# Kernel tuning notes

Measured on AMD Instinct MI355X. Metric: run time of the kernel, lower is better.

The kernel has to match this reference:

```python
import jax, jax.numpy as jnp
import numpy as np
from jax import lax

H = 1024  # hidden_size
L = 2     # num_layers


def gru_cell(x, h, Wih, Whh, bih, bhh):
    # PyTorch GRU gate order: r, z, n
    gi = x @ Wih.T + bih          # [B, 3H]
    gh = h @ Whh.T + bhh          # [B, 3H]
    ir, iz, inn = jnp.split(gi, 3, axis=-1)
    hr, hz, hn = jnp.split(gh, 3, axis=-1)
    r = jax.nn.sigmoid(ir + hr)
    z = jax.nn.sigmoid(iz + hz)
    n = jnp.tanh(inn + r * hn)
    return (1.0 - z) * n + z * h


def stacked_step(h, x_t, layers):
    # h: [L, B, H]; x_t: [B, in]; layers: list of (Wih, Whh, bih, bhh)
    hs = []
    inp = x_t
    for l, (Wih, Whh, bih, bhh) in enumerate(layers):
        hl = gru_cell(inp, h[l], Wih, Whh, bih, bhh)
        hs.append(hl)
        inp = hl
    return jnp.stack(hs), inp  # new hidden stack, top-layer output


def run_gru_seq(x_seq, h0, layers):
    # x_seq: [B, S, in] -> scan over time
    def step(h, x_t):
        h_new, out = stacked_step(h, x_t, layers)
        return h_new, out
    h_final, outs = lax.scan(step, h0, jnp.transpose(x_seq, (1, 0, 2)))
    return outs[-1], h_final  # last-timestep top-layer output [B, H]


def setup_inputs() -> dict:
    key = jax.random.key(0)
    ks = jax.random.split(key, 10)
    B, S = 128, 256

    def xavier(k, shape):
        fan_out, fan_in = shape
        std = np.sqrt(2.0 / (fan_in + fan_out))
        return jax.random.normal(k, shape, dtype=jnp.float32) * std

    inp = {
        "x": jax.random.normal(ks[0], (B, S), dtype=jnp.float32),
        "h0": jax.random.uniform(ks[1], (L, B, H), dtype=jnp.float32) * 0.01,
        "Wih0": xavier(ks[2], (3 * H, 1)),
        "Whh0": xavier(ks[3], (3 * H, H)),
        "bih0": jnp.zeros((3 * H,), jnp.float32),
        "bhh0": jnp.zeros((3 * H,), jnp.float32),
        "Wih1": xavier(ks[4], (3 * H, H)),
        "Whh1": xavier(ks[5], (3 * H, H)),
        "bih1": jnp.zeros((3 * H,), jnp.float32),
        "bhh1": jnp.zeros((3 * H,), jnp.float32),
        "fc_w": jax.random.uniform(ks[6], (1, H), jnp.float32, -1.0 / np.sqrt(H), 1.0 / np.sqrt(H)),
        "fc_b": jax.random.uniform(ks[7], (1,), jnp.float32, -1.0 / np.sqrt(H), 1.0 / np.sqrt(H)),
        "forcast_length": 8,
    }
    return inp


def reference(x, h0, Wih0, Whh0, bih0, bhh0, Wih1, Whh1, bih1, bhh1, fc_w, fc_b, forcast_length):
    layers = [(Wih0, Whh0, bih0, bhh0), (Wih1, Whh1, bih1, bhh1)]

    # forecast step i=0: full conditioning sequence
    out0, h = run_gru_seq(x[..., None], h0, layers)   # [B, H], [L, B, H]
    y0 = out0 @ fc_w.T + fc_b                          # [B, 1]

    def fstep(carry, _):
        xc, hc = carry                                 # xc: [B, 1]
        h_new, out = stacked_step(hc, xc, layers)
        y = out @ fc_w.T + fc_b                        # [B, 1]
        return (y, h_new), y[:, 0]

    (y_last, h_final), ys = lax.scan(fstep, (y0, h), None, length=forcast_length - 1)
    forcast_out = jnp.concatenate([y0[:, 0][None, :], ys], axis=0)  # [F, B]
    return jnp.mean(forcast_out, axis=0), h_final
```

## Files before the change

kernel.cpp:

```cpp
#include <hip/hip_runtime.h>

#define NB 128
#define NH 1024
#define NS 256
#define NF 8
#define NBLK 192
#define NTH 512
#define AG  __HIP_MEMORY_SCOPE_AGENT

#define GLOBL 0
#define RELL  64
#define INITL 128
#define XCNT  192
#define XARR  512
#define XCPY  1024

typedef _Float16 half_t;
typedef _Float16 f16x8 __attribute__((ext_vector_type(8)));
typedef float f32x4 __attribute__((ext_vector_type(4)));
typedef unsigned long long u64;

struct GP {
    const float *x, *hin, *Wih0, *Whh0, *bih0, *bhh0, *Wih1, *Whh1, *bih1, *bhh1, *fcw, *fcb;
    float *gib0, *gib1, *ys, *out;
    half_t *h0b0, *h0b1, *h1b0, *h1b1;
    char *reg;
    unsigned *bar;
};

__device__ __forceinline__ float fast_sigmoid(float x) { return 1.0f / (1.0f + __expf(-x)); }
__device__ __forceinline__ float fast_tanh(float x) {
    float e = __expf(2.0f * x);
    return (e - 1.0f) / (e + 1.0f);
}

__device__ __forceinline__ u64 ldu64(const void* p) {
    return __hip_atomic_load((const u64*)p, __ATOMIC_RELAXED, AG);
}
__device__ __forceinline__ void stu64(void* p, u64 v) {
    __hip_atomic_store((u64*)p, v, __ATOMIC_RELAXED, AG);
}
__device__ __forceinline__ float ldf32(const float* p) {
    return __hip_atomic_load(p, __ATOMIC_RELAXED, AG);
}
__device__ __forceinline__ unsigned aadd(unsigned* p, unsigned v) {
    return __hip_atomic_fetch_add(p, v, __ATOMIC_RELAXED, AG);
}
__device__ __forceinline__ unsigned ald(const unsigned* p) {
    return __hip_atomic_load(p, __ATOMIC_RELAXED, AG);
}

__device__ __forceinline__ void l2add(unsigned* p, unsigned v) {
    asm volatile("global_atomic_add %0, %1, off" :: "v"(p), "v"(v) : "memory");
}
__device__ __forceinline__ unsigned l2add_rtn(unsigned* p, unsigned v) {
    unsigned ret;
    asm volatile("global_atomic_add %0, %1, %2, off sc0\n\ts_waitcnt vmcnt(0)"
                 : "=v"(ret) : "v"(p), "v"(v) : "memory");
    return ret;
}

__global__ void k_init(const float* __restrict__ hin, half_t* __restrict__ h0h,
                       half_t* __restrict__ h1h, const float* __restrict__ fcb,
                       float* __restrict__ ys) {
    int i = blockIdx.x * 256 + threadIdx.x;
    h0h[i] = (half_t)hin[i];
    h1h[i] = (half_t)hin[NB * NH + i];
    if (blockIdx.x == 0) {
        float fb = fcb[0];
        for (int j = threadIdx.x; j < NF * NB; j += 256) ys[j] = fb;
    }
}

__global__ __launch_bounds__(NTH)
void k_gru(GP p) {
    extern __shared__ char lds[];
    const int tid = threadIdx.x;
    const int l   = tid & 63;
    const int wv  = tid >> 6;
    const int bid = blockIdx.x;
    const int role = (bid < 64) ? 0 : (bid < 128 ? 1 : 2);
    const int bc   = bid & 63;
    const int colbase = bc * 16;
    float* hl  = (float*)(lds + 98304);
    int* meta  = (int*)(lds + 106496);
    unsigned* bar = p.bar;

    {
        const float* Wsrc = (role == 0) ? p.Whh0 : ((role == 1) ? p.Wih1 : p.Whh1);
        for (int i = tid; i < 12288; i += NTH) {
            int row = i >> 8, j = i & 255;
            int g = row >> 4, r = row & 15;
            float4 v = *(const float4*)(Wsrc + (size_t)(g * NH + colbase + r) * NH + j * 4);
            union { half_t h[4]; uint2 u; } cv;
            cv.h[0] = (half_t)v.x; cv.h[1] = (half_t)v.y;
            cv.h[2] = (half_t)v.z; cv.h[3] = (half_t)v.w;
            *(uint2*)(lds + (row * 2048 + ((j * 8) ^ ((row & 7) << 4)))) = cv.u;
        }
        if (role != 1) {
            const float* hsrc = p.hin + (role == 2 ? NB * NH : 0);
            for (int i = tid; i < NB * 16; i += NTH) {
                int b = i >> 4, cl = i & 15;
                hl[i] = hsrc[(size_t)b * NH + colbase + cl];
            }
        }
    }

    if (tid == 0) {
        unsigned x;
        asm volatile("s_getreg_b32 %0, hwreg(HW_REG_XCC_ID)" : "=s"(x));
        x &= 7;
        unsigned r = aadd(bar + XCNT + x * 32, 1u);
        asm volatile("s_waitcnt vmcnt(0)" ::: "memory");
        aadd(bar + INITL, 1u);
        while (ald(bar + INITL) < NBLK) __builtin_amdgcn_s_sleep(1);
        int nn = 0, cnt = 0;
        for (int k = 0; k < 8; ++k) {
            unsigned c = ald(bar + XCNT + k * 32);
            if (c) ++cnt;
            if (k == (int)x) nn = (int)c;
        }
        meta[0] = (int)x; meta[1] = (int)r; meta[2] = nn; meta[3] = cnt;
    }
    __syncthreads();
    const int xcd_  = meta[0];
    const int rank_ = meta[1];
    const int n_    = meta[2];
    const int nx_   = meta[3];

    const int cloc = l & 15;
    const int c = colbase + cloc;
    float bi_[3] = {0,0,0}, bh_[3] = {0,0,0}, wx_[3] = {0,0,0}, fcwv = 0.f;
    if (role == 0) {
        #pragma unroll
        for (int g = 0; g < 3; ++g) {
            bi_[g] = p.bih0[g * NH + c]; bh_[g] = p.bhh0[g * NH + c];
            wx_[g] = p.Wih0[g * NH + c];
        }
    } else if (role == 2) {
        #pragma unroll
        for (int g = 0; g < 3; ++g) {
            bi_[g] = p.bih1[g * NH + c]; bh_[g] = p.bhh1[g * NH + c];
        }
        fcwv = p.fcw[c];
    }

    const int rbase[3] = { cloc * 2048, (16 + cloc) * 2048, (32 + cloc) * 2048 };
    const int rmask = (cloc & 7) << 4;
    const int kb0 = (l >> 4) << 4;
    const int arow = wv * 16 + cloc;
    const int b0base = wv * 16 + ((l >> 4) << 2);
    const int aloff = (l >> 4) * 2048 + arow * 16;

    auto gbar = [&](unsigned t) {
        __syncthreads();
        if (tid == 0) {
            l2add(bar + XARR + xcd_ * 32, 1u);
            if (rank_ == 0) {
                while (l2add_rtn(bar + XARR + xcd_ * 32, 0u) < (unsigned)n_ * t)
                    __builtin_amdgcn_s_sleep(1);
                unsigned old = aadd(bar + GLOBL, 1u);
                if (old == (unsigned)nx_ * t - 1u) aadd(bar + RELL, 1u);
            }
            while (ald(bar + RELL) < t) __builtin_amdgcn_s_sleep(1);
        }
        __syncthreads();
        asm volatile("buffer_inv" ::: "memory");
    };

    auto xcopy = [&](const half_t* h0s, const half_t* h1s, int slot) {
        char* dst = p.reg + ((size_t)(xcd_ * 2 + slot)) * 524288;
        for (int idx = rank_ * 512 + tid; idx < 32768; idx += n_ * 512) {
            int which = idx >> 14, kq = (idx >> 7) & 127, row = idx & 127;
            const half_t* s = (which ? h1s : h0s) + row * 1024 + kq * 8;
            union { u64 u[2]; uint4 v; } t;
            t.u[0] = ldu64(s);
            t.u[1] = ldu64(s + 4);
            *(uint4*)(dst + which * 262144 + (size_t)(kq * 128 + row) * 16) = t.v;
        }
    };
    auto csync = [&](unsigned ct) {
        __syncthreads();
        if (tid == 0) {
            l2add(bar + XCPY + xcd_ * 32, 1u);
            while (l2add_rtn(bar + XCPY + xcd_ * 32, 0u) < (unsigned)n_ * ct)
                __builtin_amdgcn_s_sleep(1);
        }
        __syncthreads();
    };

    auto do_gemm = [&](const char* regA, f32x4 (&acc)[3]) {
        const char* ap = regA + aloff;
        #pragma unroll 8
        for (int ks = 0; ks < 32; ++ks) {
            f16x8 a = *(const f16x8*)(ap + (size_t)ks * 8192);
            int kb = ks * 64 + kb0;
            #pragma unroll
            for (int g = 0; g < 3; ++g) {
                f16x8 bf = *(const f16x8*)(lds + rbase[g] + (kb ^ rmask));
                acc[g] = __builtin_amdgcn_mfma_f32_16x16x32_f16(a, bf, acc[g], 0, 0, 0);
            }
        }
    };

    auto pack_store_h = [&](half_t* hw, int b, float hn) {
        unsigned v = (unsigned)__builtin_bit_cast(unsigned short, (half_t)hn);
        unsigned o = __shfl_xor(v, 1);
        unsigned pair = (l & 1) ? (o | (v << 16)) : (v | (o << 16));
        unsigned p2 = __shfl_xor(pair, 2);
        u64 quad = (l & 2) ? (((u64)pair << 32) | p2) : ((u64)pair | ((u64)p2 << 32));
        if ((l & 3) == 0) stu64(hw + (size_t)b * NH + (c & ~3), quad);
    };

    auto l0_epi = [&](const float xv[4], f32x4 (&acc)[3], half_t* hw) {
        #pragma unroll
        for (int q = 0; q < 4; ++q) {
            int b = b0base + q;
            float gh0 = acc[0][q] + bh_[0];
            float gh1 = acc[1][q] + bh_[1];
            float gh2 = acc[2][q] + bh_[2];
            float r_ = fast_sigmoid(xv[q] * wx_[0] + bi_[0] + gh0);
            float z_ = fast_sigmoid(xv[q] * wx_[1] + bi_[1] + gh1);
            float n_2 = fast_tanh(xv[q] * wx_[2] + bi_[2] + r_ * gh2);
            float hp = hl[b * 16 + cloc];
            float hn = (1.0f - z_) * n_2 + z_ * hp;
            hl[b * 16 + cloc] = hn;
            pack_store_h(hw, b, hn);
        }
    };

    auto gi_epi = [&](f32x4 (&acc)[3], float* gw) {
        #pragma unroll
        for (int g = 0; g < 3; ++g) {
            union { f32x4 v; u64 u[2]; } t; t.v = acc[g];
            float* dst = gw + ((size_t)g * NH + c) * NB + b0base;
            stu64(dst, t.u[0]);
            stu64(dst + 2, t.u[1]);
        }
    };

    auto gh_epi = [&](f32x4 (&acc)[3], const f32x4 gv[3], half_t* hw, float* ydst) {
        float hn4[4];
        #pragma unroll
        for (int q = 0; q < 4; ++q) {
            int b = b0base + q;
            float gh0 = acc[0][q] + bh_[0];
            float gh1 = acc[1][q] + bh_[1];
            float gh2 = acc[2][q] + bh_[2];
            float r_ = fast_sigmoid(gv[0][q] + bi_[0] + gh0);
            float z_ = fast_sigmoid(gv[1][q] + bi_[1] + gh1);
            float n_2 = fast_tanh(gv[2][q] + bi_[2] + r_ * gh2);
            float hp = hl[b * 16 + cloc];
            float hn = (1.0f - z_) * n_2 + z_ * hp;
            hl[b * 16 + cloc] = hn;
            hn4[q] = hn;
            pack_store_h(hw, b, hn);
        }
        if (ydst) {
            float s0 = hn4[0] * fcwv, s1 = hn4[1] * fcwv, s2 = hn4[2] * fcwv, s3 = hn4[3] * fcwv;
            #pragma unroll
            for (int m = 1; m < 16; m <<= 1) {
                s0 += __shfl_xor(s0, m); s1 += __shfl_xor(s1, m);
                s2 += __shfl_xor(s2, m); s3 += __shfl_xor(s3, m);
            }
            if (cloc == 0) {
                atomicAdd(ydst + b0base, s0);
                atomicAdd(ydst + b0base + 1, s1);
                atomicAdd(ydst + b0base + 2, s2);
                atomicAdd(ydst + b0base + 3, s3);
            }
        }
    };

    auto load_gi = [&](const float* gr, f32x4 (&gv)[3]) {
        #pragma unroll
        for (int g = 0; g < 3; ++g) {
            union { f32x4 v; u64 u[2]; } t;
            const float* src = gr + ((size_t)g * NH + c) * NB + b0base;
            t.u[0] = ldu64(src);
            t.u[1] = ldu64(src + 2);
            gv[g] = t.v;
        }
    };

    unsigned tgt = 0, ctgt = 0;
    int cur0 = 0, cur1 = 0, gcur = 0;
    f32x4 zero4 = {0.f, 0.f, 0.f, 0.f};

    auto COPY = [&]() {
        ++ctgt;
        int slot = (int)(ctgt & 1);
        xcopy(cur0 ? p.h0b1 : p.h0b0, cur1 ? p.h1b1 : p.h1b0, slot);
        csync(ctgt);
        return p.reg + ((size_t)(xcd_ * 2 + slot)) * 524288;
    };

    for (int ph = 0; ph < NS + 2; ++ph) {
        const char* regB = COPY();
        if (role == 0 && ph < NS) {
            float xv[4];
            #pragma unroll
            for (int q = 0; q < 4; ++q) xv[q] = ldf32(p.x + (size_t)(b0base + q) * NS + ph);
            f32x4 acc[3] = {zero4, zero4, zero4};
            do_gemm(regB, acc);
            l0_epi(xv, acc, cur0 ? p.h0b0 : p.h0b1);
        } else if (role == 1 && ph >= 1 && ph <= NS) {
            f32x4 acc[3] = {zero4, zero4, zero4};
            do_gemm(regB, acc);
            gi_epi(acc, gcur ? p.gib0 : p.gib1);
        } else if (role == 2 && ph >= 2) {
            f32x4 gv[3];
            load_gi(gcur ? p.gib1 : p.gib0, gv);
            f32x4 acc[3] = {zero4, zero4, zero4};
            do_gemm(regB + 262144, acc);
            gh_epi(acc, gv, cur1 ? p.h1b0 : p.h1b1, (ph == NS + 1) ? p.ys : nullptr);
        }
        ++tgt; gbar(tgt);
        if (ph < NS) cur0 ^= 1;
        if (ph >= 1 && ph <= NS) gcur ^= 1;
        if (ph >= 2) cur1 ^= 1;
    }

    for (int i = 1; i < NF; ++i) {
        const char* regB = COPY();
        if (role == 0) {
            float xv[4];
            #pragma unroll
            for (int q = 0; q < 4; ++q) xv[q] = ldf32(p.ys + (i - 1) * NB + b0base + q);
            f32x4 acc[3] = {zero4, zero4, zero4};
            do_gemm(regB, acc);
            l0_epi(xv, acc, cur0 ? p.h0b0 : p.h0b1);
        }
        ++tgt; gbar(tgt); cur0 ^= 1;

        regB = COPY();
        if (role == 1) {
            f32x4 acc[3] = {zero4, zero4, zero4};
            do_gemm(regB, acc);
            gi_epi(acc, gcur ? p.gib0 : p.gib1);
        }
        ++tgt; gbar(tgt); gcur ^= 1;

        regB = COPY();
        if (role == 2) {
            f32x4 gv[3];
            load_gi(gcur ? p.gib1 : p.gib0, gv);
            f32x4 acc[3] = {zero4, zero4, zero4};
            do_gemm(regB + 262144, acc);
            gh_epi(acc, gv, cur1 ? p.h1b0 : p.h1b1, p.ys + i * NB);
        }
        ++tgt; gbar(tgt); cur1 ^= 1;
    }

    if (bid == 0 && tid < NB) {
        float s = 0.0f;
        #pragma unroll
        for (int k = 0; k < NF; ++k) s += ldf32(p.ys + k * NB + tid);
        p.out[tid] = s * 0.125f;
    }
    if (role != 1) {
        float* ob = p.out + NB + (role == 2 ? (size_t)NB * NH : 0);
        for (int i = tid; i < NB * 16; i += NTH) {
            int b = i >> 4, cl = i & 15;
            ob[(size_t)b * NH + colbase + cl] = hl[i];
        }
    }
}

extern "C" void kernel_launch(void* const* d_in, const int* in_sizes, int n_in,
                              void* d_out, int out_size, void* d_ws, size_t ws_size,
                              hipStream_t stream)
{
    GP p;
    p.x    = (const float*)d_in[0];
    p.hin  = (const float*)d_in[1];
    p.Wih0 = (const float*)d_in[2];
    p.Whh0 = (const float*)d_in[3];
    p.bih0 = (const float*)d_in[4];
    p.bhh0 = (const float*)d_in[5];
    p.Wih1 = (const float*)d_in[6];
    p.Whh1 = (const float*)d_in[7];
    p.bih1 = (const float*)d_in[8];
    p.bhh1 = (const float*)d_in[9];
    p.fcw  = (const float*)d_in[10];
    p.fcb  = (const float*)d_in[11];
    p.out  = (float*)d_out;

    char* ws = (char*)d_ws;
    p.bar  = (unsigned*)ws;                      ws += 8192;
    p.h0b0 = (half_t*)ws;                        ws += 262144;
    p.h0b1 = (half_t*)ws;                        ws += 262144;
    p.h1b0 = (half_t*)ws;                        ws += 262144;
    p.h1b1 = (half_t*)ws;                        ws += 262144;
    p.gib0 = (float*)ws;                         ws += 1572864;
    p.gib1 = (float*)ws;                         ws += 1572864;
    p.ys   = (float*)ws;                         ws += 4096;
    ws = (char*)(((size_t)ws + 4095) & ~(size_t)4095);
    p.reg  = ws;                                 ws += 8 * 2 * 524288;

    hipMemsetAsync(p.bar, 0, 8192, stream);
    k_init<<<512, 256, 0, stream>>>(p.hin, p.h0b0, p.h1b0, p.fcb, p.ys);

    void* args[] = { &p };
    if (hipLaunchCooperativeKernel((void*)k_gru, dim3(NBLK), dim3(NTH), args,
                                   106752, stream) != hipSuccess) {
        (void)hipGetLastError();
        k_gru<<<dim3(NBLK), dim3(NTH), 106752, stream>>>(p);
    }
}
```

Baseline: 3.316 ms.

## Restructure grid barrier release per XCD and streamline h-state staging copy

The global barrier now releases each XCD through a per-XCD counter: the XCD leader spins on the global count and then bumps a local release flag, so other blocks no longer all poll one global line. The staging copy becomes a straight linear memcpy with four batched non-temporal dwordx4 loads issued before any store, and the A-operand addressing in the GEMM is changed to match the new row-major staging layout. Loads of x and of the gi buffer are hoisted ahead of the copy and sync so their latency overlaps them. This adds explicit vmcnt waits before each barrier and assumes the buffer layout used by the GEMM is consistent with the unpermuted copy.

```diff
diff --git a/kernel.cpp b/kernel.cpp
--- a/kernel.cpp
+++ b/kernel.cpp
@@ -9,10 +9,10 @@
 #define AG  __HIP_MEMORY_SCOPE_AGENT
 
 #define GLOBL 0
-#define RELL  64
 #define INITL 128
 #define XCNT  192
 #define XARR  512
+#define XREL  768
 #define XCPY  1024
 
 typedef _Float16 half_t;
@@ -150,19 +150,24 @@
     const int kb0 = (l >> 4) << 4;
     const int arow = wv * 16 + cloc;
     const int b0base = wv * 16 + ((l >> 4) << 2);
-    const int aloff = (l >> 4) * 2048 + arow * 16;
+    const int aloff = arow * 2048 + ((l >> 4) << 4);
 
     auto gbar = [&](unsigned t) {
+        asm volatile("s_waitcnt vmcnt(0)" ::: "memory");
         __syncthreads();
         if (tid == 0) {
             l2add(bar + XARR + xcd_ * 32, 1u);
             if (rank_ == 0) {
                 while (l2add_rtn(bar + XARR + xcd_ * 32, 0u) < (unsigned)n_ * t)
                     __builtin_amdgcn_s_sleep(1);
-                unsigned old = aadd(bar + GLOBL, 1u);
-                if (old == (unsigned)nx_ * t - 1u) aadd(bar + RELL, 1u);
-            }
-            while (ald(bar + RELL) < t) __builtin_amdgcn_s_sleep(1);
+                aadd(bar + GLOBL, 1u);
+                while (aadd(bar + GLOBL, 0u) < (unsigned)nx_ * t)
+                    __builtin_amdgcn_s_sleep(1);
+                l2add(bar + XREL + xcd_ * 32, 1u);
+            } else {
+                while (l2add_rtn(bar + XREL + xcd_ * 32, 0u) < t)
+                    __builtin_amdgcn_s_sleep(1);
+            }
         }
         __syncthreads();
         asm volatile("buffer_inv" ::: "memory");
@@ -170,16 +175,28 @@
 
     auto xcopy = [&](const half_t* h0s, const half_t* h1s, int slot) {
         char* dst = p.reg + ((size_t)(xcd_ * 2 + slot)) * 524288;
-        for (int idx = rank_ * 512 + tid; idx < 32768; idx += n_ * 512) {
-            int which = idx >> 14, kq = (idx >> 7) & 127, row = idx & 127;
-            const half_t* s = (which ? h1s : h0s) + row * 1024 + kq * 8;
-            union { u64 u[2]; uint4 v; } t;
-            t.u[0] = ldu64(s);
-            t.u[1] = ldu64(s + 4);
-            *(uint4*)(dst + which * 262144 + (size_t)(kq * 128 + row) * 16) = t.v;
-        }
+        const int base = rank_ * NTH + tid;
+        const int stride = n_ * NTH;
+        uint4 v0, v1, v2, v3;
+        int i0 = base, i1 = base + stride, i2 = base + 2 * stride, i3 = base + 3 * stride;
+        const char* s0 = (i0 < 16384) ? (const char*)h0s + (size_t)i0 * 16 : (const char*)h1s + (size_t)(i0 - 16384) * 16;
+        const char* s1 = (i1 < 16384) ? (const char*)h0s + (size_t)i1 * 16 : (const char*)h1s + (size_t)(i1 - 16384) * 16;
+        const char* s2 = (i2 < 16384) ? (const char*)h0s + (size_t)i2 * 16 : (const char*)h1s + (size_t)(i2 - 16384) * 16;
+        const char* s3 = (i3 < 16384) ? (const char*)h0s + (size_t)i3 * 16 : (const char*)h1s + (size_t)(i3 - 16384) * 16;
+        if (i0 < 32768) asm volatile("global_load_dwordx4 %0, %1, off sc0 sc1" : "=v"(v0) : "v"(s0) : "memory");
+        if (i1 < 32768) asm volatile("global_load_dwordx4 %0, %1, off sc0 sc1" : "=v"(v1) : "v"(s1) : "memory");
+        if (i2 < 32768) asm volatile("global_load_dwordx4 %0, %1, off sc0 sc1" : "=v"(v2) : "v"(s2) : "memory");
+        if (i3 < 32768) asm volatile("global_load_dwordx4 %0, %1, off sc0 sc1" : "=v"(v3) : "v"(s3) : "memory");
+        __builtin_amdgcn_sched_barrier(0);
+        asm volatile("s_waitcnt vmcnt(0)" ::: "memory");
+        __builtin_amdgcn_sched_barrier(0);
+        if (i0 < 32768) *(uint4*)(dst + (size_t)i0 * 16) = v0;
+        if (i1 < 32768) *(uint4*)(dst + (size_t)i1 * 16) = v1;
+        if (i2 < 32768) *(uint4*)(dst + (size_t)i2 * 16) = v2;
+        if (i3 < 32768) *(uint4*)(dst + (size_t)i3 * 16) = v3;
     };
     auto csync = [&](unsigned ct) {
+        asm volatile("s_waitcnt vmcnt(0)" ::: "memory");
         __syncthreads();
         if (tid == 0) {
             l2add(bar + XCPY + xcd_ * 32, 1u);
@@ -193,7 +210,7 @@
         const char* ap = regA + aloff;
         #pragma unroll 8
         for (int ks = 0; ks < 32; ++ks) {
-            f16x8 a = *(const f16x8*)(ap + (size_t)ks * 8192);
+            f16x8 a = *(const f16x8*)(ap + ks * 64);
             int kb = ks * 64 + kb0;
             #pragma unroll
             for (int g = 0; g < 3; ++g) {
@@ -296,11 +313,16 @@
     };
 
     for (int ph = 0; ph < NS + 2; ++ph) {
+        float xv[4];
+        f32x4 gv[3];
+        if (role == 0 && ph < NS) {
+            #pragma unroll
+            for (int q = 0; q < 4; ++q) xv[q] = p.x[(size_t)(b0base + q) * NS + ph];
+        } else if (role == 2 && ph >= 2) {
+            load_gi(gcur ? p.gib1 : p.gib0, gv);
+        }
         const char* regB = COPY();
         if (role == 0 && ph < NS) {
-            float xv[4];
-            #pragma unroll
-            for (int q = 0; q < 4; ++q) xv[q] = ldf32(p.x + (size_t)(b0base + q) * NS + ph);
             f32x4 acc[3] = {zero4, zero4, zero4};
             do_gemm(regB, acc);
             l0_epi(xv, acc, cur0 ? p.h0b0 : p.h0b1);
@@ -309,8 +331,6 @@
             do_gemm(regB, acc);
             gi_epi(acc, gcur ? p.gib0 : p.gib1);
         } else if (role == 2 && ph >= 2) {
-            f32x4 gv[3];
-            load_gi(gcur ? p.gib1 : p.gib0, gv);
             f32x4 acc[3] = {zero4, zero4, zero4};
             do_gemm(regB + 262144, acc);
             gh_epi(acc, gv, cur1 ? p.h1b0 : p.h1b1, (ph == NS + 1) ? p.ys : nullptr);
@@ -322,11 +342,13 @@
     }
 
     for (int i = 1; i < NF; ++i) {
+        float xv[4];
+        if (role == 0) {
+            #pragma unroll
+            for (int q = 0; q < 4; ++q) xv[q] = ldf32(p.ys + (i - 1) * NB + b0base + q);
+        }
         const char* regB = COPY();
         if (role == 0) {
-            float xv[4];
-            #pragma unroll
-            for (int q = 0; q < 4; ++q) xv[q] = ldf32(p.ys + (i - 1) * NB + b0base + q);
             f32x4 acc[3] = {zero4, zero4, zero4};
             do_gemm(regB, acc);
             l0_epi(xv, acc, cur0 ? p.h0b0 : p.h0b1);
@@ -341,13 +363,15 @@
         }
         ++tgt; gbar(tgt); gcur ^= 1;
 
-        regB = COPY();
-        if (role == 2) {
+        {
             f32x4 gv[3];
-            load_gi(gcur ? p.gib1 : p.gib0, gv);
-            f32x4 acc[3] = {zero4, zero4, zero4};
-            do_gemm(regB + 262144, acc);
-            gh_epi(acc, gv, cur1 ? p.h1b0 : p.h1b1, p.ys + i * NB);
+            if (role == 2) load_gi(gcur ? p.gib1 : p.gib0, gv);
+            regB = COPY();
+            if (role == 2) {
+                f32x4 acc[3] = {zero4, zero4, zero4};
+                do_gemm(regB + 262144, acc);
+                gh_epi(acc, gv, cur1 ? p.h1b0 : p.h1b1, p.ys + i * NB);
+            }
         }
         ++tgt; gbar(tgt); cur1 ^= 1;
     }
```

After: 3.970 ms. 19.7% more time.

## Replace fc output atomics with per-block partials and prefetch inputs before copy

Applied to the files above, without the earlier changes.

The fc projection no longer uses atomicAdd into a shared ys array. Each layer-1 block now writes its partial dot products to a per-block slot, and the layer-0 blocks reduce the 64 partials with loads and wave shuffles when they need the next input. The running mean is kept in registers instead of rereading ys at the end. The x values and the gi loads are now issued before the cross-XCD copy/sync, so their latency overlaps with it, and the GEMM unroll is raised to 16. This removes contended float atomics and the fcb init pass, at the cost of redundant partial-sum reads in every layer-0 block each forecast step.

```diff
diff --git a/kernel.cpp b/kernel.cpp
--- a/kernel.cpp
+++ b/kernel.cpp
@@ -22,7 +22,7 @@
 
 struct GP {
     const float *x, *hin, *Wih0, *Whh0, *bih0, *bhh0, *Wih1, *Whh1, *bih1, *bhh1, *fcw, *fcb;
-    float *gib0, *gib1, *ys, *out;
+    float *gib0, *gib1, *ypart, *out;
     half_t *h0b0, *h0b1, *h1b0, *h1b1;
     char *reg;
     unsigned *bar;
@@ -42,6 +42,9 @@
 }
 __device__ __forceinline__ float ldf32(const float* p) {
     return __hip_atomic_load(p, __ATOMIC_RELAXED, AG);
+}
+__device__ __forceinline__ void stf32(float* p, float v) {
+    __hip_atomic_store(p, v, __ATOMIC_RELAXED, AG);
 }
 __device__ __forceinline__ unsigned aadd(unsigned* p, unsigned v) {
     return __hip_atomic_fetch_add(p, v, __ATOMIC_RELAXED, AG);
@@ -61,15 +64,10 @@
 }
 
 __global__ void k_init(const float* __restrict__ hin, half_t* __restrict__ h0h,
-                       half_t* __restrict__ h1h, const float* __restrict__ fcb,
-                       float* __restrict__ ys) {
+                       half_t* __restrict__ h1h) {
     int i = blockIdx.x * 256 + threadIdx.x;
     h0h[i] = (half_t)hin[i];
     h1h[i] = (half_t)hin[NB * NH + i];
-    if (blockIdx.x == 0) {
-        float fb = fcb[0];
-        for (int j = threadIdx.x; j < NF * NB; j += 256) ys[j] = fb;
-    }
 }
 
 __global__ __launch_bounds__(NTH)
@@ -130,13 +128,14 @@
 
     const int cloc = l & 15;
     const int c = colbase + cloc;
-    float bi_[3] = {0,0,0}, bh_[3] = {0,0,0}, wx_[3] = {0,0,0}, fcwv = 0.f;
+    float bi_[3] = {0,0,0}, bh_[3] = {0,0,0}, wx_[3] = {0,0,0}, fcwv = 0.f, fcb_ = 0.f;
     if (role == 0) {
         #pragma unroll
         for (int g = 0; g < 3; ++g) {
             bi_[g] = p.bih0[g * NH + c]; bh_[g] = p.bhh0[g * NH + c];
             wx_[g] = p.Wih0[g * NH + c];
         }
+        fcb_ = p.fcb[0];
     } else if (role == 2) {
         #pragma unroll
         for (int g = 0; g < 3; ++g) {
@@ -170,7 +169,7 @@
 
     auto xcopy = [&](const half_t* h0s, const half_t* h1s, int slot) {
         char* dst = p.reg + ((size_t)(xcd_ * 2 + slot)) * 524288;
-        for (int idx = rank_ * 512 + tid; idx < 32768; idx += n_ * 512) {
+        for (int idx = rank_ * NTH + tid; idx < 32768; idx += n_ * NTH) {
             int which = idx >> 14, kq = (idx >> 7) & 127, row = idx & 127;
             const half_t* s = (which ? h1s : h0s) + row * 1024 + kq * 8;
             union { u64 u[2]; uint4 v; } t;
@@ -191,7 +190,7 @@
 
     auto do_gemm = [&](const char* regA, f32x4 (&acc)[3]) {
         const char* ap = regA + aloff;
-        #pragma unroll 8
+        #pragma unroll 16
         for (int ks = 0; ks < 32; ++ks) {
             f16x8 a = *(const f16x8*)(ap + (size_t)ks * 8192);
             int kb = ks * 64 + kb0;
@@ -264,10 +263,11 @@
                 s2 += __shfl_xor(s2, m); s3 += __shfl_xor(s3, m);
             }
             if (cloc == 0) {
-                atomicAdd(ydst + b0base, s0);
-                atomicAdd(ydst + b0base + 1, s1);
-                atomicAdd(ydst + b0base + 2, s2);
-                atomicAdd(ydst + b0base + 3, s3);
+                float* yp = ydst + bc * NB + b0base;
+                stf32(yp,     s0);
+                stf32(yp + 1, s1);
+                stf32(yp + 2, s2);
+                stf32(yp + 3, s3);
             }
         }
     };
@@ -283,24 +283,49 @@
         }
     };
 
+    auto reduce_y = [&](float xv[4]) {
+        float s[4];
+        #pragma unroll
+        for (int q = 0; q < 4; ++q) {
+            float t0 = ldf32(p.ypart + (cloc * 4 + 0) * NB + b0base + q);
+            float t1 = ldf32(p.ypart + (cloc * 4 + 1) * NB + b0base + q);
+            float t2 = ldf32(p.ypart + (cloc * 4 + 2) * NB + b0base + q);
+            float t3 = ldf32(p.ypart + (cloc * 4 + 3) * NB + b0base + q);
+            s[q] = (t0 + t1) + (t2 + t3);
+        }
+        #pragma unroll
+        for (int m = 1; m < 16; m <<= 1) {
+            s[0] += __shfl_xor(s[0], m); s[1] += __shfl_xor(s[1], m);
+            s[2] += __shfl_xor(s[2], m); s[3] += __shfl_xor(s[3], m);
+        }
+        #pragma unroll
+        for (int q = 0; q < 4; ++q) xv[q] = s[q] + fcb_;
+    };
+
     unsigned tgt = 0, ctgt = 0;
     int cur0 = 0, cur1 = 0, gcur = 0;
     f32x4 zero4 = {0.f, 0.f, 0.f, 0.f};
+    float ysum[4] = {0.f, 0.f, 0.f, 0.f};
 
     auto COPY = [&]() {
         ++ctgt;
         int slot = (int)(ctgt & 1);
         xcopy(cur0 ? p.h0b1 : p.h0b0, cur1 ? p.h1b1 : p.h1b0, slot);
         csync(ctgt);
-        return p.reg + ((size_t)(xcd_ * 2 + slot)) * 524288;
+        return (const char*)(p.reg + (size_t)(xcd_ * 2 + slot) * 524288);
     };
 
     for (int ph = 0; ph < NS + 2; ++ph) {
+        float xv[4];
+        f32x4 gv[3];
+        if (role == 0 && ph < NS) {
+            #pragma unroll
+            for (int q = 0; q < 4; ++q) xv[q] = p.x[(size_t)(b0base + q) * NS + ph];
+        } else if (role == 2 && ph >= 2) {
+            load_gi(gcur ? p.gib1 : p.gib0, gv);
+        }
         const char* regB = COPY();
         if (role == 0 && ph < NS) {
-            float xv[4];
-            #pragma unroll
-            for (int q = 0; q < 4; ++q) xv[q] = ldf32(p.x + (size_t)(b0base + q) * NS + ph);
             f32x4 acc[3] = {zero4, zero4, zero4};
             do_gemm(regB, acc);
             l0_epi(xv, acc, cur0 ? p.h0b0 : p.h0b1);
@@ -309,11 +334,9 @@
             do_gemm(regB, acc);
             gi_epi(acc, gcur ? p.gib0 : p.gib1);
         } else if (role == 2 && ph >= 2) {
-            f32x4 gv[3];
-            load_gi(gcur ? p.gib1 : p.gib0, gv);
             f32x4 acc[3] = {zero4, zero4, zero4};
             do_gemm(regB + 262144, acc);
-            gh_epi(acc, gv, cur1 ? p.h1b0 : p.h1b1, (ph == NS + 1) ? p.ys : nullptr);
+            gh_epi(acc, gv, cur1 ? p.h1b0 : p.h1b1, (ph == NS + 1) ? p.ypart : nullptr);
         }
         ++tgt; gbar(tgt);
         if (ph < NS) cur0 ^= 1;
@@ -322,11 +345,14 @@
     }
 
     for (int i = 1; i < NF; ++i) {
+        float xv[4];
+        if (role == 0) {
+            reduce_y(xv);
+            #pragma unroll
+            for (int q = 0; q < 4; ++q) ysum[q] += xv[q];
+        }
         const char* regB = COPY();
         if (role == 0) {
-            float xv[4];
-            #pragma unroll
-            for (int q = 0; q < 4; ++q) xv[q] = ldf32(p.ys + (i - 1) * NB + b0base + q);
             f32x4 acc[3] = {zero4, zero4, zero4};
             do_gemm(regB, acc);
             l0_epi(xv, acc, cur0 ? p.h0b0 : p.h0b1);
@@ -341,22 +367,27 @@
         }
         ++tgt; gbar(tgt); gcur ^= 1;
 
-        regB = COPY();
-        if (role == 2) {
+        {
             f32x4 gv[3];
-            load_gi(gcur ? p.gib1 : p.gib0, gv);
-            f32x4 acc[3] = {zero4, zero4, zero4};
-            do_gemm(regB + 262144, acc);
-            gh_epi(acc, gv, cur1 ? p.h1b0 : p.h1b1, p.ys + i * NB);
+            if (role == 2) load_gi(gcur ? p.gib1 : p.gib0, gv);
+            regB = COPY();
+            if (role == 2) {
+                f32x4 acc[3] = {zero4, zero4, zero4};
+                do_gemm(regB + 262144, acc);
+                gh_epi(acc, gv, cur1 ? p.h1b0 : p.h1b1, p.ypart);
+            }
         }
         ++tgt; gbar(tgt); cur1 ^= 1;
     }
 
-    if (bid == 0 && tid < NB) {
-        float s = 0.0f;
-        #pragma unroll
-        for (int k = 0; k < NF; ++k) s += ldf32(p.ys + k * NB + tid);
-        p.out[tid] = s * 0.125f;
+    if (role == 0) {
+        float y7[4];
+        reduce_y(y7);
+        if (bid == 0 && cloc == 0) {
+            #pragma unroll
+            for (int q = 0; q < 4; ++q)
+                p.out[b0base + q] = (ysum[q] + y7[q]) * 0.125f;
+        }
     }
     if (role != 1) {
         float* ob = p.out + NB + (role == 2 ? (size_t)NB * NH : 0);
@@ -387,19 +418,19 @@
     p.out  = (float*)d_out;
 
     char* ws = (char*)d_ws;
-    p.bar  = (unsigned*)ws;                      ws += 8192;
-    p.h0b0 = (half_t*)ws;                        ws += 262144;
-    p.h0b1 = (half_t*)ws;                        ws += 262144;
-    p.h1b0 = (half_t*)ws;                        ws += 262144;
-    p.h1b1 = (half_t*)ws;                        ws += 262144;
-    p.gib0 = (float*)ws;                         ws += 1572864;
-    p.gib1 = (float*)ws;                         ws += 1572864;
-    p.ys   = (float*)ws;                         ws += 4096;
+    p.bar   = (unsigned*)ws;                     ws += 8192;
+    p.h0b0  = (half_t*)ws;                       ws += 262144;
+    p.h0b1  = (half_t*)ws;                       ws += 262144;
+    p.h1b0  = (half_t*)ws;                       ws += 262144;
+    p.h1b1  = (half_t*)ws;                       ws += 262144;
+    p.gib0  = (float*)ws;                        ws += 1572864;
+    p.gib1  = (float*)ws;                        ws += 1572864;
+    p.ypart = (float*)ws;                        ws += 32768;
     ws = (char*)(((size_t)ws + 4095) & ~(size_t)4095);
-    p.reg  = ws;                                 ws += 8 * 2 * 524288;
+    p.reg   = ws;                                ws += 8 * 2 * 524288;
 
     hipMemsetAsync(p.bar, 0, 8192, stream);
-    k_init<<<512, 256, 0, stream>>>(p.hin, p.h0b0, p.h1b0, p.fcb, p.ys);
+    k_init<<<512, 256, 0, stream>>>(p.hin, p.h0b0, p.h1b0);
 
     void* args[] = { &p };
     if (hipLaunchCooperativeKernel((void*)k_gru, dim3(NBLK), dim3(NTH), args,
```

New measurement: 3.721 ms. 1.12x slower.
